# Kernel optimization log

Measured on AMD Instinct MI355X. Metric: run time of the kernel, lower is better.

## Reference

```python
import jax, jax.numpy as jnp
import numpy as np

B, T, U = 1024, 256, 256  # batch, timesteps, units (= input_dim)


def setup_inputs() -> dict:
    key = jax.random.key(0)
    ks = jax.random.split(key, 8)
    g = lambda k, shape: (jax.random.normal(k, shape, dtype=jnp.float32)
                          * np.float32(np.sqrt(2.0 / sum(shape if len(shape) > 1 else (shape[0], 1)))))
    return {
        "inputs": jax.random.normal(ks[0], (B, T, U), dtype=jnp.float32),
        "embedding_kernel": g(ks[1], (U, U)),
        "state_kernel": g(ks[2], (U, U)),
        "bias": g(ks[3], (U,)),
        "length_kernel": g(ks[4], (U, 1)),
        "rnn_state_kernel": g(ks[5], (U, 3 * U)),
        "rnn_embedding_kernel": g(ks[6], (U, 3 * U)),
        "rnn_newin_kernel": g(ks[7], (U, 3 * U)),
    }


def reference(inputs, embedding_kernel, state_kernel, bias, length_kernel,
              rnn_state_kernel, rnn_embedding_kernel, rnn_newin_kernel):
    u = state_kernel.shape[0]
    b = inputs.shape[0]

    def step(carry, x):
        state, s1, s2 = carry                       # each (B, U)
        query = state @ state_kernel                # (B, U)
        value = jnp.stack([s1, s2, x], axis=1)      # (B, 3, U) -- 3 memory slots
        emb = jnp.einsum('bsu,uv->bsv', value, embedding_kernel)
        act = jnp.tanh(emb + query[:, None, :] + bias)          # (B, 3, U)
        scores = jnp.einsum('bsu,u->bs', act, length_kernel[:, 0])  # (B, 3)
        prob = jax.nn.softmax(scores, axis=1)
        attention_out = jnp.einsum('bsu,bs->bu', value, prob)   # (B, U)

        gs = state @ rnn_state_kernel               # (B, 3U)
        ge = attention_out @ rnn_embedding_kernel   # (B, 3U)
        gn = x @ rnn_newin_kernel                   # (B, 3U)
        u_p = jax.nn.sigmoid(gs[:, :u] + ge[:, :u] + gn[:, :u])
        r_p = jax.nn.sigmoid(gs[:, u:2*u] + ge[:, u:2*u] + gn[:, u:2*u])
        cand = jnp.tanh(r_p * gs[:, 2*u:] + ge[:, 2*u:] + gn[:, 2*u:])
        step_out = (1.0 - u_p) * state + u_p * cand
        # state update mirrors Keras: [step_out, states[2], step_in]
        return (step_out, s2, x), None

    init = (jnp.zeros((b, u), inputs.dtype),
            jnp.zeros((b, u), inputs.dtype),
            jnp.zeros((b, u), inputs.dtype))
    xs = jnp.swapaxes(inputs, 0, 1)  # (T, B, U)
    (last_out, _, _), _ = jax.lax.scan(step, init, xs)
    return last_out  # (B, U) -- K.rnn's last_output
```

## Files before the change

### kernel.cpp

```cpp
#include <hip/hip_runtime.h>


typedef _Float16 f16;
typedef _Float16 f16x8 __attribute__((ext_vector_type(8)));
typedef _Float16 f16x4 __attribute__((ext_vector_type(4)));
typedef float f32x4 __attribute__((ext_vector_type(4)));

static __device__ __forceinline__ f32x4 mfma16(f16x8 a, f16x8 b, f32x4 c){
  return __builtin_amdgcn_mfma_f32_16x16x32_f16(a, b, c, 0, 0, 0);
}
static __device__ __forceinline__ float sigmoid_f(float x){
  return 1.0f / (1.0f + __expf(-x));
}
static __device__ __forceinline__ float tanh_f(float x){
  float e = __expf(2.0f * x);
  return 1.0f - 2.0f / (e + 1.0f);
}
static __device__ __forceinline__ void lgkm_barrier(){
  asm volatile("s_waitcnt lgkmcnt(0)" ::: "memory");
  __builtin_amdgcn_s_barrier();
}

__global__ void cast_x_kernel(const float* __restrict__ X, f16* __restrict__ Xh){
  size_t e = ((size_t)blockIdx.x * 256 + threadIdx.x) * 8;
  f32x4 v0 = *(const f32x4*)(X + e);
  f32x4 v1 = *(const f32x4*)(X + e + 4);
  f16x8 h;
  #pragma unroll
  for (int j = 0; j < 8; ++j) h[j] = (f16)((j < 4) ? v0[j] : v1[j-4]);
  *(f16x8*)(Xh + e) = h;
}

__global__ void cast_w_kernel(const float* __restrict__ EK, const float* __restrict__ RE,
    const float* __restrict__ NW, const float* __restrict__ SK, const float* __restrict__ RS,
    f16* __restrict__ WcatT, f16* __restrict__ WsrF){
  int tid = blockIdx.x * 256 + threadIdx.x;
  if (tid < 458752){
    int n = tid >> 8, k = tid & 255;
    float v;
    if (n < 256)       v = EK[k*256 + n];
    else if (n < 1024) v = RE[k*768 + (n-256)];
    else               v = NW[k*768 + (n-1024)];
    WcatT[n*256 + k] = (f16)v;
  } else {
    int idx = tid - 458752;
    int e    = idx & 7;
    int lane = (idx >> 3) & 63;
    int kt   = (idx >> 9) & 7;
    int ct   = idx >> 12;
    int col  = ct*16 + (lane & 15);
    int k    = kt*32 + ((lane >> 4) & 3)*8 + e;
    float v = (col < 256) ? SK[k*256 + col] : RS[k*768 + (col-256)];
    WsrF[idx] = (f16)v;
  }
}

__global__ __launch_bounds__(256, 2) void gemm_f16_kernel(
    const f16* __restrict__ Xh, const f16* __restrict__ Bm,
    f16* __restrict__ C, int Mtiles, int t_start)
{
  __shared__ f16 As[128*64];
  __shared__ f16 Bs[128*64];
  const int NT = 14;
  const int nwg = Mtiles * NT;
  int bid = blockIdx.x, wg = bid;
  if ((nwg & 7) == 0){ int cpx = nwg >> 3; wg = (bid & 7) * cpx + (bid >> 3); }
  const int mt = wg / NT, nt = wg % NT;
  const int tsl = mt >> 3;
  const int b0  = (mt & 7) * 128;
  const int t   = t_start + tsl;
  const int n0  = nt * 128;
  const int tid = threadIdx.x;
  const int l = tid & 63, wid = tid >> 6;
  const int wr = wid >> 1, wc = wid & 1;
  const int srow = tid >> 3;
  const int scol = (tid & 7) * 8;

  const size_t ASTR = 32ull * 65536ull;
  const f16* Ab = Xh + ((size_t)(b0 + srow) * 256 + t) * 256 + scol;
  const f16* Bb = Bm + ((size_t)(n0 + srow)) * 256 + scol;

  f16x8 ra[4], rb[4];
  #pragma unroll
  for (int j = 0; j < 4; ++j){
    ra[j] = *(const f16x8*)(Ab + (size_t)j * ASTR);
    rb[j] = *(const f16x8*)(Bb + (size_t)j * 32 * 256);
  }

  f32x4 acc[4][4];
  #pragma unroll
  for (int mi = 0; mi < 4; ++mi)
    #pragma unroll
    for (int ni = 0; ni < 4; ++ni)
      acc[mi][ni] = (f32x4){0.f,0.f,0.f,0.f};

  for (int kt = 0; kt < 4; ++kt){
    #pragma unroll
    for (int j = 0; j < 4; ++j){
      int row = srow + j*32;
      int e = (row*64 + scol) ^ ((row & 7) << 3);
      *(f16x8*)&As[e] = ra[j];
      *(f16x8*)&Bs[e] = rb[j];
    }
    __syncthreads();
    if (kt < 3){
      #pragma unroll
      for (int j = 0; j < 4; ++j){
        ra[j] = *(const f16x8*)(Ab + (kt+1)*64 + (size_t)j * ASTR);
        rb[j] = *(const f16x8*)(Bb + (kt+1)*64 + (size_t)j * 32 * 256);
      }
    }
    #pragma unroll
    for (int kk = 0; kk < 2; ++kk){
      f16x8 af[4], bfr[4];
      #pragma unroll
      for (int mi = 0; mi < 4; ++mi){
        int row = wr*64 + mi*16 + (l & 15);
        int e = (row*64 + kk*32 + (l >> 4)*8) ^ ((row & 7) << 3);
        af[mi] = *(const f16x8*)&As[e];
      }
      #pragma unroll
      for (int ni = 0; ni < 4; ++ni){
        int row = wc*64 + ni*16 + (l & 15);
        int e = (row*64 + kk*32 + (l >> 4)*8) ^ ((row & 7) << 3);
        bfr[ni] = *(const f16x8*)&Bs[e];
      }
      #pragma unroll
      for (int mi = 0; mi < 4; ++mi)
        #pragma unroll
        for (int ni = 0; ni < 4; ++ni)
          acc[mi][ni] = mfma16(af[mi], bfr[ni], acc[mi][ni]);
    }
    __syncthreads();
  }
  const size_t m0 = (size_t)mt * 128;
  #pragma unroll
  for (int mi = 0; mi < 4; ++mi){
    #pragma unroll
    for (int ni = 0; ni < 4; ++ni){
      int col = n0 + wc*64 + ni*16 + (l & 15);
      size_t row = m0 + wr*64 + mi*16 + ((l >> 4) * 4);
      #pragma unroll
      for (int j = 0; j < 4; ++j)
        C[(row + j) * 1792 + col] = (f16)acc[mi][ni][j];
    }
  }
}

__global__ __launch_bounds__(512, 1) void recurrent_kernel(
    const f16* __restrict__ P, const f16* __restrict__ WsrF,
    const float* __restrict__ bias, const float* __restrict__ Lk,
    float* __restrict__ state, float* __restrict__ out,
    int t0, int nsteps)
{
  __shared__ f16 Wl[8*8192];
  __shared__ f16 qg16[8*1032];
  __shared__ f16 stA[8*520];
  __shared__ __align__(16) float sb[256];
  __shared__ __align__(16) float sl[256];

  const int tid = threadIdx.x;
  const int l = tid & 63, w = tid >> 6;
  const int r0 = blockIdx.x * 8;
  const int arow = l & 15, agrp = l >> 4;
  const int c4 = l * 4;
  const int gb = r0 + w;
  const size_t SL = 1024ull*1792ull;
  const size_t gbo = (size_t)gb*1792;

  if (tid < 256){ sb[tid] = bias[tid]; sl[tid] = Lk[tid]; }
  for (int j = tid; j < 8*520; j += 512) stA[j] = (f16)0.f;

  const f16* const wbase = WsrF + (size_t)w*32768 + l*8;
  f16x8 Wreg[8][6];
  #pragma unroll
  for (int ct = 0; ct < 8; ++ct)
    #pragma unroll
    for (int kt = 0; kt < 6; ++kt)
      Wreg[ct][kt] = *(const f16x8*)(wbase + (ct*8 + kt)*512);
  #pragma unroll
  for (int ct = 0; ct < 8; ++ct)
    #pragma unroll
    for (int k2 = 0; k2 < 2; ++k2)
      *(f16x8*)&Wl[w*8192 + (ct*2 + k2)*512 + l*8] =
          *(const f16x8*)(wbase + (ct*8 + 6 + k2)*512);
  __syncthreads();

  f32x4 sn = *(const f32x4*)(state + (size_t)gb*256 + c4);
  f16* const sa = &stA[(l >> 3)*520 + ((((l >> 1) & 3) << 4) + w)*8 + (l & 1)*4];
  { f16x4 h; h[0]=(f16)sn[0]; h[1]=(f16)sn[1]; h[2]=(f16)sn[2]; h[3]=(f16)sn[3]; *(f16x4*)sa = h; }
  lgkm_barrier();

  for (int i = 0; i < nsteps; ++i){
    const int t = t0 + i;
    const f16* p2 = P + (size_t)(i+2)*SL + gbo;
    const f16* p1 = P + (size_t)(i+1)*SL + gbo;
    const f16* p0 = P + (size_t)(i+0)*SL + gbo;

    #pragma unroll
    for (int ct = 0; ct < 8; ++ct)
      #pragma unroll
      for (int kt = 0; kt < 6; ++kt)
        asm volatile("" : "+v"(Wreg[ct][kt]));

    const f16x4 cE2 = *(const f16x4*)(p2 + c4);
    const f16x4 cU  = *(const f16x4*)(p2 +  256 + c4);
    const f16x4 cR  = *(const f16x4*)(p2 +  512 + c4);
    const f16x4 cC  = *(const f16x4*)(p2 +  768 + c4);
    const f16x4 cNU = *(const f16x4*)(p2 + 1024 + c4);
    const f16x4 cNR = *(const f16x4*)(p2 + 1280 + c4);
    const f16x4 cNC = *(const f16x4*)(p2 + 1536 + c4);

    #pragma unroll
    for (int qtr = 0; qtr < 4; ++qtr){
      f32x4 acc[2];
      acc[0] = (f32x4){0.f,0.f,0.f,0.f};
      acc[1] = acc[0];
      #pragma unroll
      for (int kt = 0; kt < 8; ++kt){
        const f16x8 av = *(const f16x8*)&stA[kt*520 + l*8];
        #pragma unroll
        for (int c = 0; c < 2; ++c){
          const int ct = qtr*2 + c;
          f16x8 B;
          if (kt < 6) B = Wreg[ct][kt];
          else        B = *(const f16x8*)&Wl[w*8192 + (ct*2 + (kt-6))*512 + l*8];
          acc[c] = mfma16(av, B, acc[c]);
        }
      }
      if (agrp < 2){
        #pragma unroll
        for (int c = 0; c < 2; ++c){
          const int col = w*128 + (qtr*2 + c)*16 + arow;
          #pragma unroll
          for (int j = 0; j < 4; ++j)
            qg16[(agrp*4 + j)*1032 + col] = (f16)acc[c][j];
        }
      }
    }
    lgkm_barrier();

    const f16x4 E0 = *(const f16x4*)(p0 + c4);
    const f16x4 E1 = *(const f16x4*)(p1 + c4);
    const f16x4 U1 = *(const f16x4*)(p1 + 256 + c4);
    const f16x4 R1 = *(const f16x4*)(p1 + 512 + c4);
    const f16x4 C1 = *(const f16x4*)(p1 + 768 + c4);
    const f16x4 U2 = *(const f16x4*)(p0 + 256 + c4);
    const f16x4 R2 = *(const f16x4*)(p0 + 512 + c4);
    const f16x4 C2 = *(const f16x4*)(p0 + 768 + c4);

    const f16x4 qv = *(const f16x4*)&qg16[w*1032 + c4];
    const f32x4 bb = *(const f32x4*)&sb[c4];
    const f32x4 lk = *(const f32x4*)&sl[c4];
    float s0 = 0.f, s1 = 0.f, s2 = 0.f;
    #pragma unroll
    for (int j = 0; j < 4; ++j){
      const float qb = (float)qv[j] + bb[j];
      s0 += tanh_f((float)E0[j]  + qb) * lk[j];
      s1 += tanh_f((float)E1[j]  + qb) * lk[j];
      s2 += tanh_f((float)cE2[j] + qb) * lk[j];
    }
    #pragma unroll
    for (int off = 32; off; off >>= 1){
      s0 += __shfl_xor(s0, off);
      s1 += __shfl_xor(s1, off);
      s2 += __shfl_xor(s2, off);
    }
    const float mx = fmaxf(fmaxf(s0, s1), s2);
    const float x0 = __expf(s0 - mx), x1 = __expf(s1 - mx), x2 = __expf(s2 - mx);
    const float inv = 1.0f / (x0 + x1 + x2);
    const float pr0 = x0*inv, pr1 = x1*inv, pr2 = x2*inv;

    const f16x4 qu = *(const f16x4*)&qg16[w*1032 + 256 + c4];
    const f16x4 qr = *(const f16x4*)&qg16[w*1032 + 512 + c4];
    const f16x4 qc = *(const f16x4*)&qg16[w*1032 + 768 + c4];
    #pragma unroll
    for (int j = 0; j < 4; ++j){
      const float geu = pr2*(float)cU[j] + pr1*(float)U1[j] + pr0*(float)U2[j];
      const float ger = pr2*(float)cR[j] + pr1*(float)R1[j] + pr0*(float)R2[j];
      const float gec = pr2*(float)cC[j] + pr1*(float)C1[j] + pr0*(float)C2[j];
      const float up   = sigmoid_f((float)qu[j] + geu + (float)cNU[j]);
      const float rp   = sigmoid_f((float)qr[j] + ger + (float)cNR[j]);
      const float cand = tanh_f(rp*(float)qc[j] + gec + (float)cNC[j]);
      sn[j] = (1.0f - up)*sn[j] + up*cand;
    }
    { f16x4 h; h[0]=(f16)sn[0]; h[1]=(f16)sn[1]; h[2]=(f16)sn[2]; h[3]=(f16)sn[3]; *(f16x4*)sa = h; }
    if (t == 255) *(f32x4*)(out + (size_t)gb*256 + c4) = sn;
    lgkm_barrier();
  }

  *(f32x4*)(state + (size_t)gb*256 + c4) = sn;
}

extern "C" void kernel_launch(void* const* d_in, const int* in_sizes, int n_in,
                              void* d_out, int out_size, void* d_ws, size_t ws_size,
                              hipStream_t stream)
{
  const float* X  = (const float*)d_in[0];
  const float* EK = (const float*)d_in[1];
  const float* SK = (const float*)d_in[2];
  const float* BI = (const float*)d_in[3];
  const float* LK = (const float*)d_in[4];
  const float* RS = (const float*)d_in[5];
  const float* RE = (const float*)d_in[6];
  const float* NW = (const float*)d_in[7];
  float* out = (float*)d_out;
  char* ws = (char*)d_ws;

  const size_t slabB = 1024ull * 1792ull * 2ull;
  const size_t XhB   = 134217728ull;
  const size_t wB    = 917504ull + 524288ull + 1048576ull;
  int CT = 4;
  if      (ws_size >= 34ull*slabB + XhB + wB) CT = 32;
  else if (ws_size >= 18ull*slabB + XhB + wB) CT = 16;
  else if (ws_size >= 10ull*slabB + XhB + wB) CT = 8;

  f16* P = (f16*)ws;
  size_t poff = (size_t)(CT + 2) * slabB;
  f16* Xh    = (f16*)(ws + poff);
  f16* WcatT = (f16*)(ws + poff + XhB);
  f16* WsrF  = (f16*)(ws + poff + XhB + 917504ull);
  float* state = (float*)(ws + poff + XhB + 917504ull + 524288ull);

  hipMemsetAsync(state, 0, 1048576ull, stream);
  hipMemsetAsync(P, 0, 2ull*slabB, stream);
  cast_x_kernel<<<32768, 256, 0, stream>>>(X, Xh);
  cast_w_kernel<<<2816, 256, 0, stream>>>(EK, RE, NW, SK, RS, WcatT, WsrF);

  const int nch = 256 / CT;
  for (int c = 0; c < nch; ++c){
    const int t0 = c * CT;
    const int t_start  = (c == 0) ? 0 : (t0 - 2);
    const int slab_off = (c == 0) ? 2 : 0;
    const int Mtiles = (((c == 0) ? CT : (CT + 2)) * 1024) / 128;
    gemm_f16_kernel<<<Mtiles * 14, 256, 0, stream>>>(
        Xh, WcatT, P + (size_t)slab_off * 1024 * 1792, Mtiles, t_start);
    recurrent_kernel<<<128, 512, 0, stream>>>(P, WsrF, BI, LK, state, out, t0, CT);
  }
}
```

Measured before the change: 1.752 ms.

## Split recurrent batch rows into two half-groups and interleave their matmul and gate phases

Splits each block's eight batch rows into two groups of four. Each half-step runs the full MFMA pass over the shared state and writes the query/gate results for the other group into a double-buffered region, while waves 0-3 do the attention and GRU elementwise update for the current group. The goal is to hide the serial elementwise and softmax phase behind the matmul of the other group, and to drop one barrier from the critical path. In exchange the MFMA pass runs twice per timestep, once per half, and half the waves sit idle during the elementwise work.

```diff
diff --git a/kernel.cpp b/kernel.cpp
--- a/kernel.cpp
+++ b/kernel.cpp
@@ -147,101 +147,79 @@
   }
 }
 
-__global__ __launch_bounds__(512, 1) void recurrent_kernel(
-    const f16* __restrict__ P, const f16* __restrict__ WsrF,
-    const float* __restrict__ bias, const float* __restrict__ Lk,
-    float* __restrict__ state, float* __restrict__ out,
-    int t0, int nsteps)
-{
-  __shared__ f16 Wl[8*8192];
-  __shared__ f16 qg16[8*1032];
-  __shared__ f16 stA[8*520];
-  __shared__ __align__(16) float sb[256];
-  __shared__ __align__(16) float sl[256];
-
-  const int tid = threadIdx.x;
+template<int GP>
+static __device__ __forceinline__ void qg_pass(
+    f16x8 (&Wreg)[8][6], const f16* __restrict__ Wl_w,
+    const f16* __restrict__ stA_l, f16* __restrict__ qgdb, int w, int l)
+{
+  const int agrp = l >> 4, arow = l & 15;
+  f16x8 av[8];
+  #pragma unroll
+  for (int kt = 0; kt < 8; ++kt) av[kt] = *(const f16x8*)(stA_l + kt*520);
+  #pragma unroll
+  for (int qtr = 0; qtr < 4; ++qtr){
+    const int c0 = qtr*2, c1 = qtr*2 + 1;
+    f32x4 a0 = (f32x4){0.f,0.f,0.f,0.f}, a1 = a0;
+    #pragma unroll
+    for (int kt = 0; kt < 8; ++kt){
+      f16x8 B0 = (kt < 6) ? Wreg[c0][kt]
+                          : *(const f16x8*)(Wl_w + (c0*2 + (kt-6))*512 + l*8);
+      f16x8 B1 = (kt < 6) ? Wreg[c1][kt]
+                          : *(const f16x8*)(Wl_w + (c1*2 + (kt-6))*512 + l*8);
+      a0 = mfma16(av[kt], B0, a0);
+      a1 = mfma16(av[kt], B1, a1);
+    }
+    if (agrp == GP){
+      #pragma unroll
+      for (int j = 0; j < 4; ++j){
+        qgdb[GP*4128 + j*1032 + w*128 + c0*16 + arow] = (f16)a0[j];
+        qgdb[GP*4128 + j*1032 + w*128 + c1*16 + arow] = (f16)a1[j];
+      }
+    }
+  }
+}
+
+template<int G>
+static __device__ __forceinline__ void half_body(
+    int i, int t_abs, const f16* __restrict__ P, int r0, int tid,
+    f16x8 (&Wreg)[8][6], const f16* __restrict__ Wl, f16* __restrict__ qgdb,
+    f16* __restrict__ stA, const float* __restrict__ sb, const float* __restrict__ sl,
+    f32x4& sn, f16* sa, float* __restrict__ out)
+{
+  constexpr int GP = 1 - G;
   const int l = tid & 63, w = tid >> 6;
-  const int r0 = blockIdx.x * 8;
-  const int arow = l & 15, agrp = l >> 4;
   const int c4 = l * 4;
-  const int gb = r0 + w;
   const size_t SL = 1024ull*1792ull;
-  const size_t gbo = (size_t)gb*1792;
-
-  if (tid < 256){ sb[tid] = bias[tid]; sl[tid] = Lk[tid]; }
-  for (int j = tid; j < 8*520; j += 512) stA[j] = (f16)0.f;
-
-  const f16* const wbase = WsrF + (size_t)w*32768 + l*8;
-  f16x8 Wreg[8][6];
+  const f16* stA_l = stA + l*8;
+  const f16* Wl_w  = Wl + w*8192;
+
+  f16x4 E0, E1, E2, Uc, Rc, Cc, NU, NR, NC;
+  const f16 *p2 = P, *p1 = P, *p0 = P;
+  if (w < 4){
+    const size_t gbo = (size_t)(r0 + G*4 + w)*1792;
+    p2 = P + (size_t)(i+2)*SL + gbo;
+    p1 = P + (size_t)(i+1)*SL + gbo;
+    p0 = P + (size_t)(i+0)*SL + gbo;
+    E2 = *(const f16x4*)(p2 + c4);
+    E1 = *(const f16x4*)(p1 + c4);
+    E0 = *(const f16x4*)(p0 + c4);
+    Uc = *(const f16x4*)(p2 +  256 + c4);
+    Rc = *(const f16x4*)(p2 +  512 + c4);
+    Cc = *(const f16x4*)(p2 +  768 + c4);
+    NU = *(const f16x4*)(p2 + 1024 + c4);
+    NR = *(const f16x4*)(p2 + 1280 + c4);
+    NC = *(const f16x4*)(p2 + 1536 + c4);
+  }
+
   #pragma unroll
   for (int ct = 0; ct < 8; ++ct)
     #pragma unroll
     for (int kt = 0; kt < 6; ++kt)
-      Wreg[ct][kt] = *(const f16x8*)(wbase + (ct*8 + kt)*512);
-  #pragma unroll
-  for (int ct = 0; ct < 8; ++ct)
-    #pragma unroll
-    for (int k2 = 0; k2 < 2; ++k2)
-      *(f16x8*)&Wl[w*8192 + (ct*2 + k2)*512 + l*8] =
-          *(const f16x8*)(wbase + (ct*8 + 6 + k2)*512);
-  __syncthreads();
-
-  f32x4 sn = *(const f32x4*)(state + (size_t)gb*256 + c4);
-  f16* const sa = &stA[(l >> 3)*520 + ((((l >> 1) & 3) << 4) + w)*8 + (l & 1)*4];
-  { f16x4 h; h[0]=(f16)sn[0]; h[1]=(f16)sn[1]; h[2]=(f16)sn[2]; h[3]=(f16)sn[3]; *(f16x4*)sa = h; }
-  lgkm_barrier();
-
-  for (int i = 0; i < nsteps; ++i){
-    const int t = t0 + i;
-    const f16* p2 = P + (size_t)(i+2)*SL + gbo;
-    const f16* p1 = P + (size_t)(i+1)*SL + gbo;
-    const f16* p0 = P + (size_t)(i+0)*SL + gbo;
-
-    #pragma unroll
-    for (int ct = 0; ct < 8; ++ct)
-      #pragma unroll
-      for (int kt = 0; kt < 6; ++kt)
-        asm volatile("" : "+v"(Wreg[ct][kt]));
-
-    const f16x4 cE2 = *(const f16x4*)(p2 + c4);
-    const f16x4 cU  = *(const f16x4*)(p2 +  256 + c4);
-    const f16x4 cR  = *(const f16x4*)(p2 +  512 + c4);
-    const f16x4 cC  = *(const f16x4*)(p2 +  768 + c4);
-    const f16x4 cNU = *(const f16x4*)(p2 + 1024 + c4);
-    const f16x4 cNR = *(const f16x4*)(p2 + 1280 + c4);
-    const f16x4 cNC = *(const f16x4*)(p2 + 1536 + c4);
-
-    #pragma unroll
-    for (int qtr = 0; qtr < 4; ++qtr){
-      f32x4 acc[2];
-      acc[0] = (f32x4){0.f,0.f,0.f,0.f};
-      acc[1] = acc[0];
-      #pragma unroll
-      for (int kt = 0; kt < 8; ++kt){
-        const f16x8 av = *(const f16x8*)&stA[kt*520 + l*8];
-        #pragma unroll
-        for (int c = 0; c < 2; ++c){
-          const int ct = qtr*2 + c;
-          f16x8 B;
-          if (kt < 6) B = Wreg[ct][kt];
-          else        B = *(const f16x8*)&Wl[w*8192 + (ct*2 + (kt-6))*512 + l*8];
-          acc[c] = mfma16(av, B, acc[c]);
-        }
-      }
-      if (agrp < 2){
-        #pragma unroll
-        for (int c = 0; c < 2; ++c){
-          const int col = w*128 + (qtr*2 + c)*16 + arow;
-          #pragma unroll
-          for (int j = 0; j < 4; ++j)
-            qg16[(agrp*4 + j)*1032 + col] = (f16)acc[c][j];
-        }
-      }
-    }
-    lgkm_barrier();
-
-    const f16x4 E0 = *(const f16x4*)(p0 + c4);
-    const f16x4 E1 = *(const f16x4*)(p1 + c4);
+      asm volatile("" : "+v"(Wreg[ct][kt]));
+
+  qg_pass<GP>(Wreg, Wl_w, stA_l, qgdb, w, l);
+
+  if (w < 4){
     const f16x4 U1 = *(const f16x4*)(p1 + 256 + c4);
     const f16x4 R1 = *(const f16x4*)(p1 + 512 + c4);
     const f16x4 C1 = *(const f16x4*)(p1 + 768 + c4);
@@ -249,16 +227,21 @@
     const f16x4 R2 = *(const f16x4*)(p0 + 512 + c4);
     const f16x4 C2 = *(const f16x4*)(p0 + 768 + c4);
 
-    const f16x4 qv = *(const f16x4*)&qg16[w*1032 + c4];
-    const f32x4 bb = *(const f32x4*)&sb[c4];
-    const f32x4 lk = *(const f32x4*)&sl[c4];
+    const f16* qrow = qgdb + G*4128 + w*1032;
+    const f16x4 qv = *(const f16x4*)(qrow + c4);
+    const f16x4 qu = *(const f16x4*)(qrow + 256 + c4);
+    const f16x4 qr = *(const f16x4*)(qrow + 512 + c4);
+    const f16x4 qc = *(const f16x4*)(qrow + 768 + c4);
+    const f32x4 bb = *(const f32x4*)(sb + c4);
+    const f32x4 lk = *(const f32x4*)(sl + c4);
+
     float s0 = 0.f, s1 = 0.f, s2 = 0.f;
     #pragma unroll
     for (int j = 0; j < 4; ++j){
       const float qb = (float)qv[j] + bb[j];
-      s0 += tanh_f((float)E0[j]  + qb) * lk[j];
-      s1 += tanh_f((float)E1[j]  + qb) * lk[j];
-      s2 += tanh_f((float)cE2[j] + qb) * lk[j];
+      s0 += tanh_f((float)E0[j] + qb) * lk[j];
+      s1 += tanh_f((float)E1[j] + qb) * lk[j];
+      s2 += tanh_f((float)E2[j] + qb) * lk[j];
     }
     #pragma unroll
     for (int off = 32; off; off >>= 1){
@@ -271,25 +254,84 @@
     const float inv = 1.0f / (x0 + x1 + x2);
     const float pr0 = x0*inv, pr1 = x1*inv, pr2 = x2*inv;
 
-    const f16x4 qu = *(const f16x4*)&qg16[w*1032 + 256 + c4];
-    const f16x4 qr = *(const f16x4*)&qg16[w*1032 + 512 + c4];
-    const f16x4 qc = *(const f16x4*)&qg16[w*1032 + 768 + c4];
     #pragma unroll
     for (int j = 0; j < 4; ++j){
-      const float geu = pr2*(float)cU[j] + pr1*(float)U1[j] + pr0*(float)U2[j];
-      const float ger = pr2*(float)cR[j] + pr1*(float)R1[j] + pr0*(float)R2[j];
-      const float gec = pr2*(float)cC[j] + pr1*(float)C1[j] + pr0*(float)C2[j];
-      const float up   = sigmoid_f((float)qu[j] + geu + (float)cNU[j]);
-      const float rp   = sigmoid_f((float)qr[j] + ger + (float)cNR[j]);
-      const float cand = tanh_f(rp*(float)qc[j] + gec + (float)cNC[j]);
+      const float geu = pr2*(float)Uc[j] + pr1*(float)U1[j] + pr0*(float)U2[j];
+      const float ger = pr2*(float)Rc[j] + pr1*(float)R1[j] + pr0*(float)R2[j];
+      const float gec = pr2*(float)Cc[j] + pr1*(float)C1[j] + pr0*(float)C2[j];
+      const float up   = sigmoid_f((float)qu[j] + geu + (float)NU[j]);
+      const float rp   = sigmoid_f((float)qr[j] + ger + (float)NR[j]);
+      const float cand = tanh_f(rp*(float)qc[j] + gec + (float)NC[j]);
       sn[j] = (1.0f - up)*sn[j] + up*cand;
     }
     { f16x4 h; h[0]=(f16)sn[0]; h[1]=(f16)sn[1]; h[2]=(f16)sn[2]; h[3]=(f16)sn[3]; *(f16x4*)sa = h; }
-    if (t == 255) *(f32x4*)(out + (size_t)gb*256 + c4) = sn;
-    lgkm_barrier();
-  }
-
-  *(f32x4*)(state + (size_t)gb*256 + c4) = sn;
+    if (t_abs == 255){
+      *(f32x4*)(out + (size_t)(r0 + G*4 + w)*256 + c4) = sn;
+    }
+  }
+  lgkm_barrier();
+}
+
+__global__ __launch_bounds__(512, 1) void recurrent_kernel(
+    const f16* __restrict__ P, const f16* __restrict__ WsrF,
+    const float* __restrict__ bias, const float* __restrict__ Lk,
+    float* __restrict__ state, float* __restrict__ out,
+    int t0, int nsteps)
+{
+  __shared__ f16 Wl[8*8192];
+  __shared__ f16 qgdb[2*4*1032];
+  __shared__ f16 stA[8*520];
+  __shared__ __align__(16) float sb[256];
+  __shared__ __align__(16) float sl[256];
+
+  const int tid = threadIdx.x;
+  const int l = tid & 63, w = tid >> 6;
+  const int r0 = blockIdx.x * 8;
+  const int c4 = l * 4;
+
+  if (tid < 256){ sb[tid] = bias[tid]; sl[tid] = Lk[tid]; }
+  for (int j = tid; j < 8*520; j += 512) stA[j] = (f16)0.f;
+
+  const f16* const wbase = WsrF + (size_t)w*32768 + l*8;
+  f16x8 Wreg[8][6];
+  #pragma unroll
+  for (int ct = 0; ct < 8; ++ct)
+    #pragma unroll
+    for (int kt = 0; kt < 6; ++kt)
+      Wreg[ct][kt] = *(const f16x8*)(wbase + (ct*8 + kt)*512);
+  #pragma unroll
+  for (int ct = 0; ct < 8; ++ct)
+    #pragma unroll
+    for (int k2 = 0; k2 < 2; ++k2)
+      *(f16x8*)&Wl[w*8192 + (ct*2 + k2)*512 + l*8] =
+          *(const f16x8*)(wbase + (ct*8 + 6 + k2)*512);
+  __syncthreads();
+
+  f32x4 snA = (f32x4){0.f,0.f,0.f,0.f}, snB = snA;
+  f16 *saA = stA, *saB = stA;
+  if (w < 4){
+    snA = *(const f32x4*)(state + (size_t)(r0 + w)*256 + c4);
+    snB = *(const f32x4*)(state + (size_t)(r0 + 4 + w)*256 + c4);
+    saA = &stA[(l >> 3)*520 + ((((l >> 1) & 3) << 4) + w)*8 + (l & 1)*4];
+    saB = &stA[(l >> 3)*520 + ((((l >> 1) & 3) << 4) + w + 4)*8 + (l & 1)*4];
+    { f16x4 h; h[0]=(f16)snA[0]; h[1]=(f16)snA[1]; h[2]=(f16)snA[2]; h[3]=(f16)snA[3]; *(f16x4*)saA = h; }
+    { f16x4 h; h[0]=(f16)snB[0]; h[1]=(f16)snB[1]; h[2]=(f16)snB[2]; h[3]=(f16)snB[3]; *(f16x4*)saB = h; }
+  }
+  lgkm_barrier();
+
+  qg_pass<0>(Wreg, Wl + w*8192, stA + l*8, qgdb, w, l);
+  lgkm_barrier();
+
+  for (int i = 0; i < nsteps; ++i){
+    const int t_abs = t0 + i;
+    half_body<0>(i, t_abs, P, r0, tid, Wreg, Wl, qgdb, stA, sb, sl, snA, saA, out);
+    half_body<1>(i, t_abs, P, r0, tid, Wreg, Wl, qgdb, stA, sb, sl, snB, saB, out);
+  }
+
+  if (w < 4){
+    *(f32x4*)(state + (size_t)(r0 + w)*256 + c4)     = snA;
+    *(f32x4*)(state + (size_t)(r0 + 4 + w)*256 + c4) = snB;
+  }
 }
 
 extern "C" void kernel_launch(void* const* d_in, const int* in_sizes, int n_in,
```

After: 3.047 ms. +73.9%, slower.

## Fuse input fp32-to-fp16 cast into GEMM loads and restructure recurrent MFMA loop

Applied to the files above, without the earlier changes.

Removes the separate cast_x kernel and its 128MB fp16 staging buffer by having the GEMM read fp32 inputs directly and convert to fp16 in registers before the LDS store. This avoids a full extra read/write pass over the input, but the GEMM now loads twice as many bytes per A tile, and each A tile is re-read once for each of the 14 N tiles. Separately, the recurrent step computes all 8 column tiles' accumulators in one k-loop with double-buffered LDS A-fragment loads instead of four quarter passes. It also hoists the qu/qr/qc LDS reads earlier. This adds accumulator register pressure.

```diff
diff --git a/kernel.cpp b/kernel.cpp
--- a/kernel.cpp
+++ b/kernel.cpp
@@ -19,16 +19,6 @@
 static __device__ __forceinline__ void lgkm_barrier(){
   asm volatile("s_waitcnt lgkmcnt(0)" ::: "memory");
   __builtin_amdgcn_s_barrier();
-}
-
-__global__ void cast_x_kernel(const float* __restrict__ X, f16* __restrict__ Xh){
-  size_t e = ((size_t)blockIdx.x * 256 + threadIdx.x) * 8;
-  f32x4 v0 = *(const f32x4*)(X + e);
-  f32x4 v1 = *(const f32x4*)(X + e + 4);
-  f16x8 h;
-  #pragma unroll
-  for (int j = 0; j < 8; ++j) h[j] = (f16)((j < 4) ? v0[j] : v1[j-4]);
-  *(f16x8*)(Xh + e) = h;
 }
 
 __global__ void cast_w_kernel(const float* __restrict__ EK, const float* __restrict__ RE,
@@ -56,7 +46,7 @@
 }
 
 __global__ __launch_bounds__(256, 2) void gemm_f16_kernel(
-    const f16* __restrict__ Xh, const f16* __restrict__ Bm,
+    const float* __restrict__ X, const f16* __restrict__ Bm,
     f16* __restrict__ C, int Mtiles, int t_start)
 {
   __shared__ f16 As[128*64];
@@ -77,13 +67,18 @@
   const int scol = (tid & 7) * 8;
 
   const size_t ASTR = 32ull * 65536ull;
-  const f16* Ab = Xh + ((size_t)(b0 + srow) * 256 + t) * 256 + scol;
-  const f16* Bb = Bm + ((size_t)(n0 + srow)) * 256 + scol;
+  const float* Ab = X + ((size_t)(b0 + srow) * 256 + t) * 256 + scol;
+  const f16*   Bb = Bm + ((size_t)(n0 + srow)) * 256 + scol;
 
   f16x8 ra[4], rb[4];
   #pragma unroll
   for (int j = 0; j < 4; ++j){
-    ra[j] = *(const f16x8*)(Ab + (size_t)j * ASTR);
+    f32x4 v0 = *(const f32x4*)(Ab + (size_t)j * ASTR);
+    f32x4 v1 = *(const f32x4*)(Ab + (size_t)j * ASTR + 4);
+    f16x8 h;
+    #pragma unroll
+    for (int jj = 0; jj < 8; ++jj) h[jj] = (f16)((jj < 4) ? v0[jj] : v1[jj-4]);
+    ra[j] = h;
     rb[j] = *(const f16x8*)(Bb + (size_t)j * 32 * 256);
   }
 
@@ -106,7 +101,12 @@
     if (kt < 3){
       #pragma unroll
       for (int j = 0; j < 4; ++j){
-        ra[j] = *(const f16x8*)(Ab + (kt+1)*64 + (size_t)j * ASTR);
+        f32x4 v0 = *(const f32x4*)(Ab + (kt+1)*64 + (size_t)j * ASTR);
+        f32x4 v1 = *(const f32x4*)(Ab + (kt+1)*64 + (size_t)j * ASTR + 4);
+        f16x8 h;
+        #pragma unroll
+        for (int jj = 0; jj < 8; ++jj) h[jj] = (f16)((jj < 4) ? v0[jj] : v1[jj-4]);
+        ra[j] = h;
         rb[j] = *(const f16x8*)(Bb + (kt+1)*64 + (size_t)j * 32 * 256);
       }
     }
@@ -204,6 +204,29 @@
         asm volatile("" : "+v"(Wreg[ct][kt]));
 
     const f16x4 cE2 = *(const f16x4*)(p2 + c4);
+
+    f32x4 acc[8];
+    #pragma unroll
+    for (int c = 0; c < 8; ++c) acc[c] = (f32x4){0.f,0.f,0.f,0.f};
+    {
+      f16x8 av0 = *(const f16x8*)&stA[0*520 + l*8];
+      f16x8 av1 = *(const f16x8*)&stA[1*520 + l*8];
+      #pragma unroll
+      for (int kt = 0; kt < 8; ++kt){
+        const f16x8 avc = (kt & 1) ? av1 : av0;
+        if (kt < 6){
+          f16x8 nx = *(const f16x8*)&stA[(kt+2)*520 + l*8];
+          if (kt & 1) av1 = nx; else av0 = nx;
+        }
+        #pragma unroll
+        for (int ct = 0; ct < 8; ++ct){
+          f16x8 B = (kt < 6) ? Wreg[ct][kt]
+                             : *(const f16x8*)&Wl[w*8192 + (ct*2 + (kt-6))*512 + l*8];
+          acc[ct] = mfma16(avc, B, acc[ct]);
+        }
+      }
+    }
+
     const f16x4 cU  = *(const f16x4*)(p2 +  256 + c4);
     const f16x4 cR  = *(const f16x4*)(p2 +  512 + c4);
     const f16x4 cC  = *(const f16x4*)(p2 +  768 + c4);
@@ -211,31 +234,12 @@
     const f16x4 cNR = *(const f16x4*)(p2 + 1280 + c4);
     const f16x4 cNC = *(const f16x4*)(p2 + 1536 + c4);
 
-    #pragma unroll
-    for (int qtr = 0; qtr < 4; ++qtr){
-      f32x4 acc[2];
-      acc[0] = (f32x4){0.f,0.f,0.f,0.f};
-      acc[1] = acc[0];
-      #pragma unroll
-      for (int kt = 0; kt < 8; ++kt){
-        const f16x8 av = *(const f16x8*)&stA[kt*520 + l*8];
+    if (agrp < 2){
+      #pragma unroll
+      for (int ct = 0; ct < 8; ++ct){
         #pragma unroll
-        for (int c = 0; c < 2; ++c){
-          const int ct = qtr*2 + c;
-          f16x8 B;
-          if (kt < 6) B = Wreg[ct][kt];
-          else        B = *(const f16x8*)&Wl[w*8192 + (ct*2 + (kt-6))*512 + l*8];
-          acc[c] = mfma16(av, B, acc[c]);
-        }
-      }
-      if (agrp < 2){
-        #pragma unroll
-        for (int c = 0; c < 2; ++c){
-          const int col = w*128 + (qtr*2 + c)*16 + arow;
-          #pragma unroll
-          for (int j = 0; j < 4; ++j)
-            qg16[(agrp*4 + j)*1032 + col] = (f16)acc[c][j];
-        }
+        for (int j = 0; j < 4; ++j)
+          qg16[(agrp*4 + j)*1032 + w*128 + ct*16 + arow] = (f16)acc[ct][j];
       }
     }
     lgkm_barrier();
@@ -250,6 +254,9 @@
     const f16x4 C2 = *(const f16x4*)(p0 + 768 + c4);
 
     const f16x4 qv = *(const f16x4*)&qg16[w*1032 + c4];
+    const f16x4 qu = *(const f16x4*)&qg16[w*1032 + 256 + c4];
+    const f16x4 qr = *(const f16x4*)&qg16[w*1032 + 512 + c4];
+    const f16x4 qc = *(const f16x4*)&qg16[w*1032 + 768 + c4];
     const f32x4 bb = *(const f32x4*)&sb[c4];
     const f32x4 lk = *(const f32x4*)&sl[c4];
     float s0 = 0.f, s1 = 0.f, s2 = 0.f;
@@ -271,9 +278,6 @@
     const float inv = 1.0f / (x0 + x1 + x2);
     const float pr0 = x0*inv, pr1 = x1*inv, pr2 = x2*inv;
 
-    const f16x4 qu = *(const f16x4*)&qg16[w*1032 + 256 + c4];
-    const f16x4 qr = *(const f16x4*)&qg16[w*1032 + 512 + c4];
-    const f16x4 qc = *(const f16x4*)&qg16[w*1032 + 768 + c4];
     #pragma unroll
     for (int j = 0; j < 4; ++j){
       const float geu = pr2*(float)cU[j] + pr1*(float)U1[j] + pr0*(float)U2[j];
@@ -308,23 +312,20 @@
   char* ws = (char*)d_ws;
 
   const size_t slabB = 1024ull * 1792ull * 2ull;
-  const size_t XhB   = 134217728ull;
   const size_t wB    = 917504ull + 524288ull + 1048576ull;
   int CT = 4;
-  if      (ws_size >= 34ull*slabB + XhB + wB) CT = 32;
-  else if (ws_size >= 18ull*slabB + XhB + wB) CT = 16;
-  else if (ws_size >= 10ull*slabB + XhB + wB) CT = 8;
+  if      (ws_size >= 34ull*slabB + wB) CT = 32;
+  else if (ws_size >= 18ull*slabB + wB) CT = 16;
+  else if (ws_size >= 10ull*slabB + wB) CT = 8;
 
   f16* P = (f16*)ws;
   size_t poff = (size_t)(CT + 2) * slabB;
-  f16* Xh    = (f16*)(ws + poff);
-  f16* WcatT = (f16*)(ws + poff + XhB);
-  f16* WsrF  = (f16*)(ws + poff + XhB + 917504ull);
-  float* state = (float*)(ws + poff + XhB + 917504ull + 524288ull);
+  f16* WcatT = (f16*)(ws + poff);
+  f16* WsrF  = (f16*)(ws + poff + 917504ull);
+  float* state = (float*)(ws + poff + 917504ull + 524288ull);
 
   hipMemsetAsync(state, 0, 1048576ull, stream);
   hipMemsetAsync(P, 0, 2ull*slabB, stream);
-  cast_x_kernel<<<32768, 256, 0, stream>>>(X, Xh);
   cast_w_kernel<<<2816, 256, 0, stream>>>(EK, RE, NW, SK, RS, WcatT, WsrF);
 
   const int nch = 256 / CT;
@@ -334,7 +335,7 @@
     const int slab_off = (c == 0) ? 2 : 0;
     const int Mtiles = (((c == 0) ? CT : (CT + 2)) * 1024) / 128;
     gemm_f16_kernel<<<Mtiles * 14, 256, 0, stream>>>(
-        Xh, WcatT, P + (size_t)slab_off * 1024 * 1792, Mtiles, t_start);
+        X, WcatT, P + (size_t)slab_off * 1024 * 1792, Mtiles, t_start);
     recurrent_kernel<<<128, 512, 0, stream>>>(P, WsrF, BI, LK, state, out, t0, CT);
   }
 }
```

After: 1.875 ms. 1.07x slower.
